# Kernel optimization log

Hardware: AMD Instinct MI355X
Metric: run time of the kernel (lower is better)

Reference implementation:

```python
import jax, jax.numpy as jnp
import numpy as np
import itertools, math

N_QUBITS = 16
HW_K = 8
N_LAYERS = 32
BATCH = 256
N_STATES = math.comb(N_QUBITS, HW_K)  # 12870


def _list_gates():
    gates = []
    for l in range(N_LAYERS):
        gates += [(q, q + 1) for q in range(l % 2, N_QUBITS - 1, 2)]
    return gates  # 240 gates


def _build_pairs(n, k, list_gates):
    # basis of Hamming-weight-k states, indexed as in map_RBS
    basis = list(itertools.combinations(range(n), k))
    idx = {s: i for i, s in enumerate(basis)}
    cache = {}
    rows = []
    for (i, j) in list_gates:
        if (i, j) not in cache:
            others = [q for q in range(n) if q != i and q != j]
            pr = []
            for s in itertools.combinations(others, k - 1):
                a = idx[tuple(sorted(s + (i,)))]
                b = idx[tuple(sorted(s + (j,)))]
                pr.append((a, b))
            cache[(i, j)] = pr
        rows.append(cache[(i, j)])
    return np.asarray(rows, dtype=np.int32)  # [G, P, 2], P = binom(n-2, k-1)


def setup_inputs() -> dict:
    key = jax.random.key(0)
    k1, k2 = jax.random.split(key)
    gates = _list_gates()
    pairs = jnp.asarray(_build_pairs(N_QUBITS, HW_K, gates))
    input_state = jax.random.normal(k1, (BATCH, N_STATES), dtype=jnp.float32)
    angles = jax.random.uniform(k2, (len(gates),), dtype=jnp.float32)  # nn.Parameter init torch.rand
    return {"input_state": input_state, "angles": angles, "pairs": pairs}


def reference(input_state, angles, pairs):
    # Each RBS gate applies, per affected pair (i, j) of basis states:
    #   y[i] =  cos(t) x[i] + sin(t) x[j]
    #   y[j] = -sin(t) x[i] + cos(t) x[j]
    # which is exactly (cos_matrix*cos + sin_matrix*sin + id_matrix) @ x.
    def step(state, gate):
        theta, pr = gate
        ii, jj = pr[:, 0], pr[:, 1]
        xi = state[:, ii]  # [B, P]
        xj = state[:, jj]
        c, s = jnp.cos(theta), jnp.sin(theta)
        state = state.at[:, ii].set(c * xi + s * xj)
        state = state.at[:, jj].set(c * xj - s * xi)
        return state, None

    out, _ = jax.lax.scan(step, input_state, (angles, pairs))
    return out
```

## Files before the change

### kernel.cpp

```cpp
#include <hip/hip_runtime.h>
#include <stdint.h>

#define NSTATES 12870
#define NPAD    15378
#define NPAIRS  3432
#define NGATES  240
#define PERIOD  15
#define NLP     16
#define TPB     1024

#define CS_OFF      0
#define BLK_OFF     1920
#define BLK_BYTES   23760
#define PU_ROWS     792
#define W2_ROWS     924
#define W2_SUB_OFF  12672
#define BND_OFF     96960
#define M2_OFF      4032
#define M1_OFF      14112
#define PERM_OFF    120000
#define WS_NEED     145740

__device__ __constant__ uint8_t OUTPOS[4][12] = {
  {4,5,6,7,8,9,10,11,12,13,14,15},
  {0,1,2,3,8,9,10,11,12,13,14,15},
  {0,1,2,3,4,5,6,7,12,13,14,15},
  {0,1,2,3,4,5,6,7,8,9,10,11}
};
__device__ __constant__ uint8_t FREEPOS[10] = {0,1,2,5,6,9,10,13,14,15};
__device__ __constant__ uint8_t IDPOS[16] = {0,1,2,3,4,5,6,7,8,9,10,11,12,13,14,15};
__device__ __constant__ uint8_t LRANK[16] = {0,0,1,0,2,1,2,0,3,3,4,1,5,2,3,0};
__device__ __constant__ uint8_t NBT[5]  = {1,4,6,4,1};
__device__ __constant__ uint8_t PPAD[5] = {1,5,7,5,1};

__global__ __launch_bounds__(256) void prep_fused(
    const float* __restrict__ angles, uint8_t* __restrict__ ws) {
  __shared__ int C[17][9];
  __shared__ int SECB[5][5][5];
  __shared__ int ROWB[5][5][13];
  if (threadIdx.x == 0) {
    for (int n = 0; n <= 16; ++n)
      for (int k = 0; k <= 8; ++k)
        C[n][k] = (k == 0) ? 1 : ((k > n) ? 0 : C[n-1][k-1] + C[n-1][k]);
    int acc = 0;
    for (int a0 = 0; a0 < 5; ++a0)
      for (int a1 = 0; a1 < 5; ++a1)
        for (int a2 = 0; a2 < 5; ++a2) {
          SECB[a0][a1][a2] = acc;
          int a3 = 8 - a0 - a1 - a2;
          if (a3 >= 0 && a3 <= 4) acc += NBT[a0] * NBT[a1] * NBT[a2] * PPAD[a3];
        }
  }
  for (int e = threadIdx.x; e < 325; e += 256) {
    int ow = e / 25, rem = e % 25, w0 = rem / 5, w1 = rem % 5;
    int base = 0;
    for (int c0 = 0; c0 < 5; ++c0)
      for (int c1 = 0; c1 < 5; ++c1) {
        int c2 = ow - c0 - c1;
        if (c2 < 0 || c2 > 4) continue;
        if (c0 < w0 || (c0 == w0 && c1 < w1)) base += NBT[c0] * NBT[c1] * NBT[c2];
      }
    ROWB[w0][w1][ow] = base;
  }
  __syncthreads();

  auto permof = [&](uint32_t mask) -> int {
    int g0 = mask & 15, g1 = (mask >> 4) & 15, g2 = (mask >> 8) & 15, g3 = (mask >> 12) & 15;
    int w0 = __popc(g0), w1 = __popc(g1), w2 = __popc(g2), w3 = __popc(g3);
    return SECB[w0][w1][w2] +
           ((LRANK[g0] * NBT[w1] + LRANK[g1]) * NBT[w2] + LRANK[g2]) * PPAD[w3] + LRANK[g3];
  };
  auto rowof = [&](int b, uint32_t mo) -> int {
    int wsx[3], lsx[3], ii = 0;
    for (int a = 0; a < 4; ++a) if (a != b) {
      int g = (mo >> (4 * a)) & 15;
      wsx[ii] = __popc(g); lsx[ii] = LRANK[g]; ++ii;
    }
    int outw = wsx[0] + wsx[1] + wsx[2];
    return ROWB[wsx[0]][wsx[1]][outw] +
           (lsx[0] * NBT[wsx[1]] + lsx[1]) * NBT[wsx[2]] + lsx[2];
  };
  auto unrank_mask = [&](int n, int k, int r, const uint8_t* pos) -> uint32_t {
    uint32_t m = 0; int v = 0;
    for (int i = 0; i < k; ++i) {
      for (;;) { int cnt = C[n - 1 - v][k - 1 - i]; if (r < cnt) break; r -= cnt; ++v; }
      m |= 1u << pos[v]; ++v;
    }
    return m;
  };

  int u = blockIdx.x * 256 + threadIdx.x;
  if (u < 10032) {
    int b = u / 2508, r = u % 2508;
    int p0 = 4 * b;
    uint32_t bmask = 0xFu << p0;
    uint8_t* blk = ws + BLK_OFF + b * BLK_BYTES;
    if (r < PU_ROWS) {
      uint32_t mo = unrank_mask(12, 7, r, OUTPOS[b]);
      int row = rowof(b, mo);
      uint32_t m0 = permof(mo | (1u << (p0 + 0)));
      uint32_t m1 = permof(mo | (1u << (p0 + 1)));
      uint32_t m2 = permof(mo | (1u << (p0 + 2)));
      uint32_t m3 = permof(mo | (1u << (p0 + 3)));
      uint32_t* pu = (uint32_t*)blk + (size_t)row * 4;
      pu[0] = m0 | (m1 << 16); pu[1] = m2 | (m3 << 16);
    } else if (r < PU_ROWS + W2_ROWS) {
      int o = r - PU_ROWS;
      uint32_t mo = unrank_mask(12, 6, o, OUTPOS[b]);
      int row = rowof(b, mo);
      const uint32_t pat[6] = {0x3u, 0x5u, 0x9u, 0x6u, 0xAu, 0xCu};
      uint32_t k0 = permof(mo | (pat[0] << p0)), k1 = permof(mo | (pat[1] << p0));
      uint32_t k2 = permof(mo | (pat[2] << p0)), k3 = permof(mo | (pat[3] << p0));
      uint32_t k4 = permof(mo | (pat[4] << p0)), k5 = permof(mo | (pat[5] << p0));
      uint32_t* w2 = (uint32_t*)(blk + W2_SUB_OFF) + (size_t)row * 3;
      w2[0] = k0 | (k1 << 16); w2[1] = k2 | (k3 << 16); w2[2] = k4 | (k5 << 16);
    } else {
      int o = r - PU_ROWS - W2_ROWS;
      uint32_t mo = unrank_mask(12, 5, o, OUTPOS[b]);
      int row = rowof(b, mo);
      uint32_t j0 = permof(mo | (bmask ^ (1u << (p0 + 0))));
      uint32_t j1 = permof(mo | (bmask ^ (1u << (p0 + 1))));
      uint32_t j2 = permof(mo | (bmask ^ (1u << (p0 + 2))));
      uint32_t j3 = permof(mo | (bmask ^ (1u << (p0 + 3))));
      uint32_t* pu = (uint32_t*)blk + (size_t)row * 4;
      pu[2] = j0 | (j1 << 16); pu[3] = j2 | (j3 << 16);
    }
  } else if (u < 13776) {
    int v = u - 10032;
    uint8_t* bnd = ws + BND_OFF;
    const uint32_t XL[3] = {1u << 3, 1u << 7, 1u << 11};
    const uint32_t XB[3] = {(1u<<3)|(1u<<4), (1u<<7)|(1u<<8), (1u<<11)|(1u<<12)};
    if (v < 252) {
      uint32_t mo = unrank_mask(10, 5, v, FREEPOS);
      uint32_t rep = mo | XL[0] | XL[1] | XL[2];
      uint32_t mm[8];
      for (int beta = 0; beta < 8; ++beta) {
        uint32_t m = rep;
        if (beta & 1) m ^= XB[0];
        if (beta & 2) m ^= XB[1];
        if (beta & 4) m ^= XB[2];
        mm[beta] = permof(m);
      }
      uint32_t* o = (uint32_t*)bnd + (size_t)v * 4;
      o[0] = mm[0] | (mm[1] << 16); o[1] = mm[2] | (mm[3] << 16);
      o[2] = mm[4] | (mm[5] << 16); o[3] = mm[6] | (mm[7] << 16);
    } else if (v < 1512) {
      int q = v - 252, cls = q / 420, o2 = q % 420;
      int gA = (cls == 2) ? 1 : 0;
      int gB = (cls == 0) ? 1 : 2;
      int gC = 3 - gA - gB;
      int vv = (o2 < 210) ? 0 : 1, oo = vv ? o2 - 210 : o2;
      uint32_t mo = unrank_mask(10, 6 - 2 * vv, oo, FREEPOS);
      uint32_t rep = mo | XL[gA] | XL[gB] | (vv ? XB[gC] : 0u);
      uint32_t mm[4];
      for (int beta = 0; beta < 4; ++beta) {
        uint32_t m = rep;
        if (beta & 1) m ^= XB[gA];
        if (beta & 2) m ^= XB[gB];
        mm[beta] = permof(m);
      }
      uint32_t* o = (uint32_t*)(bnd + M2_OFF + (size_t)cls * 3360) + (size_t)o2 * 2;
      o[0] = mm[0] | (mm[1] << 16); o[1] = mm[2] | (mm[3] << 16);
    } else {
      int q = v - 1512, cls = q / 744, o2 = q % 744;
      int ia = (cls == 0) ? 1 : 0;
      int ib = (cls == 2) ? 1 : 2;
      int v1, v2, f, oo;
      if      (o2 < 120) { v1 = 0; v2 = 0; f = 7; oo = o2; }
      else if (o2 < 372) { v1 = 0; v2 = 1; f = 5; oo = o2 - 120; }
      else if (o2 < 624) { v1 = 1; v2 = 0; f = 5; oo = o2 - 372; }
      else               { v1 = 1; v2 = 1; f = 3; oo = o2 - 624; }
      uint32_t mo = unrank_mask(10, f, oo, FREEPOS);
      uint32_t rep = mo | XL[cls] | (v1 ? XB[ia] : 0u) | (v2 ? XB[ib] : 0u);
      uint32_t m0 = permof(rep), m1 = permof(rep ^ XB[cls]);
      *((uint32_t*)(bnd + M1_OFF + (size_t)cls * 2976) + o2) = m0 | (m1 << 16);
    }
  } else if (u < 14016) {
    int g = u - 13776;
    float t = angles[g];
    ((float2*)(ws + CS_OFF))[g] = make_float2(cosf(t), sinf(t));
  } else if (u < 14016 + NSTATES) {
    int r = u - 14016;
    uint32_t mask = unrank_mask(16, 8, r, IDPOS);
    ((uint16_t*)(ws + PERM_OFF))[r] = (uint16_t)permof(mask);
  }
}

__device__ __forceinline__ void rot(float& rx, float& ry, const float2 cs) {
  float nx = fmaf(cs.x, rx, cs.y * ry);
  float ny = fmaf(cs.x, ry, -cs.y * rx);
  rx = nx; ry = ny;
}
__device__ __forceinline__ float lds_ld(const float* st, uint32_t boff) {
  return *(const float*)((const char*)st + boff);
}
__device__ __forceinline__ void lds_st(float* st, uint32_t boff, float v) {
  *(float*)((char*)st + boff) = v;
}

__global__ __launch_bounds__(TPB) void rbs_fused(
    const float* __restrict__ in, const uint8_t* __restrict__ ws,
    float* __restrict__ out) {
  __shared__ float st[NPAD];
  __shared__ float2 csl[NGATES];
  const int tid = threadIdx.x;
  const size_t row = blockIdx.x;
  const uint16_t* __restrict__ perm16 = (const uint16_t*)(ws + PERM_OFF);

  { const float* src = in + row * NSTATES;
    for (int i = tid; i < NSTATES; i += TPB) st[perm16[i]] = src[i]; }
  if (tid < NGATES) csl[tid] = ((const float2*)(ws + CS_OFF))[tid];

  const uint8_t* blkbase = ws + BLK_OFF;
  const uint8_t* bnd = ws + BND_OFF;
  const int w2id = (tid < 692) ? (tid + 232) : ((tid >= 792) ? (tid - 792) : -1);

  uint32_t o_i[4][4], o_j[4][4], o_k[4][6];
  if (tid < PU_ROWS) {
#pragma unroll
    for (int b = 0; b < 4; ++b) {
      uint4 mu = ((const uint4*)(blkbase + b * BLK_BYTES))[tid];
      o_i[b][0] = (mu.x & 0xffffu) << 2; o_i[b][1] = (mu.x >> 16) << 2;
      o_i[b][2] = (mu.y & 0xffffu) << 2; o_i[b][3] = (mu.y >> 16) << 2;
      o_j[b][0] = (mu.z & 0xffffu) << 2; o_j[b][1] = (mu.z >> 16) << 2;
      o_j[b][2] = (mu.w & 0xffffu) << 2; o_j[b][3] = (mu.w >> 16) << 2;
    }
  }
  if (w2id >= 0) {
#pragma unroll
    for (int b = 0; b < 4; ++b) {
      const uint32_t* p = (const uint32_t*)(blkbase + b * BLK_BYTES + W2_SUB_OFF) + (size_t)w2id * 3;
      uint32_t w0 = p[0], w1 = p[1], w2v = p[2];
      o_k[b][0] = (w0 & 0xffffu) << 2; o_k[b][1] = (w0 >> 16) << 2;
      o_k[b][2] = (w1 & 0xffffu) << 2; o_k[b][3] = (w1 >> 16) << 2;
      o_k[b][4] = (w2v & 0xffffu) << 2; o_k[b][5] = (w2v >> 16) << 2;
    }
  }
  uint4 bd[4];
#pragma unroll
  for (int k = 0; k < 4; ++k) {
    int u = tid + k * 1024;
    bd[k] = make_uint4(0u, 0u, 0u, 0u);
    if (u < 252) {
      bd[k] = ((const uint4*)bnd)[u];
    } else if (u < 1512) {
      int q = u - 252, cls = q / 420, o = q % 420;
      uint2 m = *(const uint2*)(bnd + M2_OFF + (size_t)cls * 3360 + (size_t)o * 8);
      bd[k].x = m.x; bd[k].y = m.y;
    } else if (u < 3744) {
      int q = u - 1512, cls = q / 744, o = q % 744;
      bd[k].x = *((const uint32_t*)(bnd + M1_OFF + (size_t)cls * 2976) + o);
    }
  }
  __syncthreads();

#pragma unroll 1
  for (int t = 0; t < NLP; ++t) {
    const int g0 = t * PERIOD;
#pragma unroll
    for (int b = 0; b < 4; ++b) {
      const float2 a1 = csl[g0 + 2 * b];
      const float2 a2 = csl[g0 + 2 * b + 1];
      const float2 a3 = csl[g0 + 8 + 2 * b];
      if (tid < PU_ROWS) {
        float x0 = lds_ld(st, o_i[b][0]), x1 = lds_ld(st, o_i[b][1]);
        float x2 = lds_ld(st, o_i[b][2]), x3 = lds_ld(st, o_i[b][3]);
        rot(x0, x1, a1); rot(x2, x3, a2); rot(x1, x2, a3);
        lds_st(st, o_i[b][0], x0); lds_st(st, o_i[b][1], x1);
        lds_st(st, o_i[b][2], x2); lds_st(st, o_i[b][3], x3);
        float y0 = lds_ld(st, o_j[b][0]), y1 = lds_ld(st, o_j[b][1]);
        float y2 = lds_ld(st, o_j[b][2]), y3 = lds_ld(st, o_j[b][3]);
        rot(y1, y0, a1); rot(y3, y2, a2); rot(y2, y1, a3);
        lds_st(st, o_j[b][0], y0); lds_st(st, o_j[b][1], y1);
        lds_st(st, o_j[b][2], y2); lds_st(st, o_j[b][3], y3);
      }
      if (w2id >= 0) {
        float z0 = lds_ld(st, o_k[b][0]), z1 = lds_ld(st, o_k[b][1]);
        float z2 = lds_ld(st, o_k[b][2]), z3 = lds_ld(st, o_k[b][3]);
        float z4 = lds_ld(st, o_k[b][4]), z5 = lds_ld(st, o_k[b][5]);
        rot(z1, z3, a1); rot(z2, z4, a1);
        rot(z1, z2, a2); rot(z3, z4, a2);
        rot(z0, z1, a3); rot(z4, z5, a3);
        lds_st(st, o_k[b][0], z0); lds_st(st, o_k[b][1], z1);
        lds_st(st, o_k[b][2], z2); lds_st(st, o_k[b][3], z3);
        lds_st(st, o_k[b][4], z4); lds_st(st, o_k[b][5], z5);
      }
      __syncthreads();
    }
    const float2 c0 = csl[g0 + 9], c1 = csl[g0 + 11], c2 = csl[g0 + 13];
#pragma unroll
    for (int k = 0; k < 4; ++k) {
      int u = tid + k * 1024;
      if (u >= 3744) break;
      uint4 d = bd[k];
      if (u < 252) {
        uint32_t e0 = (d.x & 0xffffu) << 2, e1 = (d.x >> 16) << 2;
        uint32_t e2 = (d.y & 0xffffu) << 2, e3 = (d.y >> 16) << 2;
        uint32_t e4 = (d.z & 0xffffu) << 2, e5 = (d.z >> 16) << 2;
        uint32_t e6 = (d.w & 0xffffu) << 2, e7 = (d.w >> 16) << 2;
        float x0 = lds_ld(st, e0), x1 = lds_ld(st, e1), x2 = lds_ld(st, e2), x3 = lds_ld(st, e3);
        float x4 = lds_ld(st, e4), x5 = lds_ld(st, e5), x6 = lds_ld(st, e6), x7 = lds_ld(st, e7);
        rot(x0, x1, c0); rot(x2, x3, c0); rot(x4, x5, c0); rot(x6, x7, c0);
        rot(x0, x2, c1); rot(x1, x3, c1); rot(x4, x6, c1); rot(x5, x7, c1);
        rot(x0, x4, c2); rot(x1, x5, c2); rot(x2, x6, c2); rot(x3, x7, c2);
        lds_st(st, e0, x0); lds_st(st, e1, x1); lds_st(st, e2, x2); lds_st(st, e3, x3);
        lds_st(st, e4, x4); lds_st(st, e5, x5); lds_st(st, e6, x6); lds_st(st, e7, x7);
      } else if (u < 1512) {
        int cls = (u - 252) / 420;
        float2 cA = (cls == 2) ? c1 : c0;
        float2 cB = (cls == 0) ? c1 : c2;
        uint32_t e0 = (d.x & 0xffffu) << 2, e1 = (d.x >> 16) << 2;
        uint32_t e2 = (d.y & 0xffffu) << 2, e3 = (d.y >> 16) << 2;
        float x0 = lds_ld(st, e0), x1 = lds_ld(st, e1), x2 = lds_ld(st, e2), x3 = lds_ld(st, e3);
        rot(x0, x1, cA); rot(x2, x3, cA);
        rot(x0, x2, cB); rot(x1, x3, cB);
        lds_st(st, e0, x0); lds_st(st, e1, x1); lds_st(st, e2, x2); lds_st(st, e3, x3);
      } else {
        int cls = (u - 1512) / 744;
        float2 cg = (cls == 0) ? c0 : ((cls == 1) ? c1 : c2);
        uint32_t e0 = (d.x & 0xffffu) << 2, e1 = (d.x >> 16) << 2;
        float x0 = lds_ld(st, e0), x1 = lds_ld(st, e1);
        rot(x0, x1, cg);
        lds_st(st, e0, x0); lds_st(st, e1, x1);
      }
    }
    __syncthreads();
  }

  { float* dst = out + row * NSTATES;
    for (int i = tid; i < NSTATES; i += TPB) dst[i] = st[perm16[i]]; }
}

__global__ __launch_bounds__(TPB) void rbs_raw(
    const float* __restrict__ in, const int* __restrict__ pairs_raw,
    const float* __restrict__ angles, float* __restrict__ out) {
  __shared__ float st[NSTATES];
  __shared__ float2 csl[NGATES];
  const int tid = threadIdx.x;
  const size_t row = blockIdx.x;
  const float* src = in + row * NSTATES;
  for (int i = tid; i < NSTATES; i += TPB) st[i] = src[i];
  for (int i = tid; i < NGATES; i += TPB) {
    float t = angles[i];
    csl[i] = make_float2(cosf(t), sinf(t));
  }
  __syncthreads();
  for (int g = 0; g < NGATES; ++g) {
    const float c = csl[g].x, s = csl[g].y;
    for (int p = tid; p < NPAIRS; p += TPB) {
      int2 ab = ((const int2*)pairs_raw)[(size_t)g * NPAIRS + p];
      float xi = st[ab.x], xj = st[ab.y];
      st[ab.x] = fmaf(c, xi, s * xj);
      st[ab.y] = fmaf(c, xj, -s * xi);
    }
    __syncthreads();
  }
  float* dst = out + row * NSTATES;
  for (int i = tid; i < NSTATES; i += TPB) dst[i] = st[i];
}

extern "C" void kernel_launch(void* const* d_in, const int* in_sizes, int n_in,
                              void* d_out, int out_size, void* d_ws, size_t ws_size,
                              hipStream_t stream) {
  const float* in = (const float*)d_in[0];
  const float* angles = (const float*)d_in[1];
  const int* pairs = (const int*)d_in[2];
  float* out = (float*)d_out;

  if (d_ws != nullptr && ws_size >= WS_NEED) {
    uint8_t* ws = (uint8_t*)d_ws;
    const int total = 14016 + NSTATES;
    prep_fused<<<(total + 255) / 256, 256, 0, stream>>>(angles, ws);
    rbs_fused<<<256, TPB, 0, stream>>>(in, ws, out);
  } else {
    rbs_raw<<<256, TPB, 0, stream>>>(in, pairs, angles, out);
  }
}
```

Baseline: 97.43 us.

## Fuse two 4-qubit blocks per pass with strided padded layout units

The per-block processing of the four 4-qubit groups (four passes, each with its own barrier) is replaced by two passes, each jointly mixing a pair of blocks (01, then 23). It uses a new padded LDS layout where the third axis is padded so each unit's addresses come from a base plus stride. Index tables shrink from per-element 16-bit offsets to one base/stride word per unit, which removes most workspace traffic and register-held offsets and halves the barriers in this phase. In exchange, the LDS footprint grows to about 73 KB of dynamic shared memory, and a deep branch tree dispatches 21 templated unit shapes with uneven per-thread work, which adds divergence.

```diff
diff --git a/kernel.cpp b/kernel.cpp
--- a/kernel.cpp
+++ b/kernel.cpp
@@ -2,42 +2,38 @@
 #include <stdint.h>
 
 #define NSTATES 12870
-#define NPAD    15378
-#define NPAIRS  3432
+#define NPAD2   18376
 #define NGATES  240
 #define PERIOD  15
 #define NLP     16
 #define TPB     1024
+#define NPAIRU  858
 
 #define CS_OFF      0
-#define BLK_OFF     1920
-#define BLK_BYTES   23760
-#define PU_ROWS     792
-#define W2_ROWS     924
-#define W2_SUB_OFF  12672
-#define BND_OFF     96960
+#define P01_OFF     1920
+#define P23_OFF     5352
+#define BND_OFF     8784
 #define M2_OFF      4032
 #define M1_OFF      14112
-#define PERM_OFF    120000
-#define WS_NEED     145740
-
-__device__ __constant__ uint8_t OUTPOS[4][12] = {
-  {4,5,6,7,8,9,10,11,12,13,14,15},
-  {0,1,2,3,8,9,10,11,12,13,14,15},
-  {0,1,2,3,4,5,6,7,12,13,14,15},
-  {0,1,2,3,4,5,6,7,8,9,10,11}
-};
+#define PERM_OFF    31824
+#define WS_NEED     57564
+#define DYNLDS      (NPAD2 * 4)
+
 __device__ __constant__ uint8_t FREEPOS[10] = {0,1,2,5,6,9,10,13,14,15};
 __device__ __constant__ uint8_t IDPOS[16] = {0,1,2,3,4,5,6,7,8,9,10,11,12,13,14,15};
 __device__ __constant__ uint8_t LRANK[16] = {0,0,1,0,2,1,2,0,3,3,4,1,5,2,3,0};
 __device__ __constant__ uint8_t NBT[5]  = {1,4,6,4,1};
 __device__ __constant__ uint8_t PPAD[5] = {1,5,7,5,1};
+__device__ __constant__ uint8_t PAX2[5] = {1,5,7,5,1};
+__device__ __constant__ uint8_t  CLSW0[21] = {0,4,0,4,0,4, 1,1,2,2,3,3, 1,1,1, 2,2,2, 3,3,3};
+__device__ __constant__ uint8_t  CLSW1[21] = {1,1,2,2,3,3, 0,4,0,4,0,4, 1,2,3, 1,2,3, 1,2,3};
+__device__ __constant__ uint16_t CLSS[22] =
+  {0,8,64,92,120,176,184,192,248,276,304,360,368,396,452,522,578,648,704,774,830,858};
 
 __global__ __launch_bounds__(256) void prep_fused(
     const float* __restrict__ angles, uint8_t* __restrict__ ws) {
   __shared__ int C[17][9];
   __shared__ int SECB[5][5][5];
-  __shared__ int ROWB[5][5][13];
   if (threadIdx.x == 0) {
     for (int n = 0; n <= 16; ++n)
       for (int k = 0; k <= 8; ++k)
@@ -48,19 +44,8 @@
         for (int a2 = 0; a2 < 5; ++a2) {
           SECB[a0][a1][a2] = acc;
           int a3 = 8 - a0 - a1 - a2;
-          if (a3 >= 0 && a3 <= 4) acc += NBT[a0] * NBT[a1] * NBT[a2] * PPAD[a3];
+          if (a3 >= 0 && a3 <= 4) acc += NBT[a0] * NBT[a1] * PAX2[a2] * PPAD[a3];
         }
-  }
-  for (int e = threadIdx.x; e < 325; e += 256) {
-    int ow = e / 25, rem = e % 25, w0 = rem / 5, w1 = rem % 5;
-    int base = 0;
-    for (int c0 = 0; c0 < 5; ++c0)
-      for (int c1 = 0; c1 < 5; ++c1) {
-        int c2 = ow - c0 - c1;
-        if (c2 < 0 || c2 > 4) continue;
-        if (c0 < w0 || (c0 == w0 && c1 < w1)) base += NBT[c0] * NBT[c1] * NBT[c2];
-      }
-    ROWB[w0][w1][ow] = base;
   }
   __syncthreads();
 
@@ -68,17 +53,7 @@
     int g0 = mask & 15, g1 = (mask >> 4) & 15, g2 = (mask >> 8) & 15, g3 = (mask >> 12) & 15;
     int w0 = __popc(g0), w1 = __popc(g1), w2 = __popc(g2), w3 = __popc(g3);
     return SECB[w0][w1][w2] +
-           ((LRANK[g0] * NBT[w1] + LRANK[g1]) * NBT[w2] + LRANK[g2]) * PPAD[w3] + LRANK[g3];
-  };
-  auto rowof = [&](int b, uint32_t mo) -> int {
-    int wsx[3], lsx[3], ii = 0;
-    for (int a = 0; a < 4; ++a) if (a != b) {
-      int g = (mo >> (4 * a)) & 15;
-      wsx[ii] = __popc(g); lsx[ii] = LRANK[g]; ++ii;
-    }
-    int outw = wsx[0] + wsx[1] + wsx[2];
-    return ROWB[wsx[0]][wsx[1]][outw] +
-           (lsx[0] * NBT[wsx[1]] + lsx[1]) * NBT[wsx[2]] + lsx[2];
+           ((LRANK[g0] * NBT[w1] + LRANK[g1]) * PAX2[w2] + LRANK[g2]) * PPAD[w3] + LRANK[g3];
   };
   auto unrank_mask = [&](int n, int k, int r, const uint8_t* pos) -> uint32_t {
     uint32_t m = 0; int v = 0;
@@ -90,43 +65,32 @@
   };
 
   int u = blockIdx.x * 256 + threadIdx.x;
-  if (u < 10032) {
-    int b = u / 2508, r = u % 2508;
-    int p0 = 4 * b;
-    uint32_t bmask = 0xFu << p0;
-    uint8_t* blk = ws + BLK_OFF + b * BLK_BYTES;
-    if (r < PU_ROWS) {
-      uint32_t mo = unrank_mask(12, 7, r, OUTPOS[b]);
-      int row = rowof(b, mo);
-      uint32_t m0 = permof(mo | (1u << (p0 + 0)));
-      uint32_t m1 = permof(mo | (1u << (p0 + 1)));
-      uint32_t m2 = permof(mo | (1u << (p0 + 2)));
-      uint32_t m3 = permof(mo | (1u << (p0 + 3)));
-      uint32_t* pu = (uint32_t*)blk + (size_t)row * 4;
-      pu[0] = m0 | (m1 << 16); pu[1] = m2 | (m3 << 16);
-    } else if (r < PU_ROWS + W2_ROWS) {
-      int o = r - PU_ROWS;
-      uint32_t mo = unrank_mask(12, 6, o, OUTPOS[b]);
-      int row = rowof(b, mo);
-      const uint32_t pat[6] = {0x3u, 0x5u, 0x9u, 0x6u, 0xAu, 0xCu};
-      uint32_t k0 = permof(mo | (pat[0] << p0)), k1 = permof(mo | (pat[1] << p0));
-      uint32_t k2 = permof(mo | (pat[2] << p0)), k3 = permof(mo | (pat[3] << p0));
-      uint32_t k4 = permof(mo | (pat[4] << p0)), k5 = permof(mo | (pat[5] << p0));
-      uint32_t* w2 = (uint32_t*)(blk + W2_SUB_OFF) + (size_t)row * 3;
-      w2[0] = k0 | (k1 << 16); w2[1] = k2 | (k3 << 16); w2[2] = k4 | (k5 << 16);
+  if (u < 2 * NPAIRU) {
+    const bool is01 = (u < NPAIRU);
+    const int uu = is01 ? u : u - NPAIRU;
+    int c = 0;
+    while (c < 20 && uu >= (int)CLSS[c + 1]) ++c;
+    int r = uu - CLSS[c];
+    const int wa = CLSW0[c], wb = CLSW1[c];
+    const int W = 8 - wa - wb;
+    int wc = 0, wd = 0, lc = 0, ld = 0;
+    for (wc = 0; wc <= 4; ++wc) {
+      wd = W - wc; if (wd < 0 || wd > 4) continue;
+      int n = NBT[wc] * NBT[wd];
+      if (r < n) { lc = r / NBT[wd]; ld = r % NBT[wd]; break; }
+      r -= n;
+    }
+    if (is01) {
+      int base = SECB[wa][wb][wc] + lc * PPAD[wd] + ld;
+      int strd = PAX2[wc] * PPAD[wd];
+      ((uint32_t*)(ws + P01_OFF))[uu] = (uint32_t)base | ((uint32_t)strd << 16);
     } else {
-      int o = r - PU_ROWS - W2_ROWS;
-      uint32_t mo = unrank_mask(12, 5, o, OUTPOS[b]);
-      int row = rowof(b, mo);
-      uint32_t j0 = permof(mo | (bmask ^ (1u << (p0 + 0))));
-      uint32_t j1 = permof(mo | (bmask ^ (1u << (p0 + 1))));
-      uint32_t j2 = permof(mo | (bmask ^ (1u << (p0 + 2))));
-      uint32_t j3 = permof(mo | (bmask ^ (1u << (p0 + 3))));
-      uint32_t* pu = (uint32_t*)blk + (size_t)row * 4;
-      pu[2] = j0 | (j1 << 16); pu[3] = j2 | (j3 << 16);
-    }
-  } else if (u < 13776) {
-    int v = u - 10032;
+      int base = SECB[wc][wd][wa] + (lc * NBT[wd] + ld) * PAX2[wa] * PPAD[wb];
+      int pstr = PPAD[wb];
+      ((uint32_t*)(ws + P23_OFF))[uu] = (uint32_t)base | ((uint32_t)pstr << 16);
+    }
+  } else if (u < 2 * NPAIRU + 3744) {
+    int v = u - 2 * NPAIRU;
     uint8_t* bnd = ws + BND_OFF;
     const uint32_t XL[3] = {1u << 3, 1u << 7, 1u << 11};
     const uint32_t XB[3] = {(1u<<3)|(1u<<4), (1u<<7)|(1u<<8), (1u<<11)|(1u<<12)};
@@ -175,12 +139,12 @@
       uint32_t m0 = permof(rep), m1 = permof(rep ^ XB[cls]);
       *((uint32_t*)(bnd + M1_OFF + (size_t)cls * 2976) + o2) = m0 | (m1 << 16);
     }
-  } else if (u < 14016) {
-    int g = u - 13776;
+  } else if (u < 2 * NPAIRU + 3744 + NGATES) {
+    int g = u - (2 * NPAIRU + 3744);
     float t = angles[g];
     ((float2*)(ws + CS_OFF))[g] = make_float2(cosf(t), sinf(t));
-  } else if (u < 14016 + NSTATES) {
-    int r = u - 14016;
+  } else if (u < 2 * NPAIRU + 3744 + NGATES + NSTATES) {
+    int r = u - (2 * NPAIRU + 3744 + NGATES);
     uint32_t mask = unrank_mask(16, 8, r, IDPOS);
     ((uint16_t*)(ws + PERM_OFF))[r] = (uint16_t)permof(mask);
   }
@@ -198,10 +162,92 @@
   *(float*)((char*)st + boff) = v;
 }
 
-__global__ __launch_bounds__(TPB) void rbs_fused(
+template<int W, int S>
+__device__ __forceinline__ void mix_axis(float* x, const float2 a1, const float2 a2, const float2 a3) {
+  if constexpr (W == 1) {
+    rot(x[0], x[S], a1); rot(x[2*S], x[3*S], a2); rot(x[S], x[2*S], a3);
+  } else if constexpr (W == 2) {
+    rot(x[S], x[2*S], a1);   rot(x[3*S], x[4*S], a1);
+    rot(x[S], x[3*S], a2);   rot(x[2*S], x[4*S], a2);
+    rot(x[0], x[S], a3);     rot(x[4*S], x[5*S], a3);
+  } else if constexpr (W == 3) {
+    rot(x[2*S], x[3*S], a1); rot(x[0], x[S], a2); rot(x[S], x[2*S], a3);
+  }
+}
+
+template<int KA, int KB>
+__device__ __forceinline__ void do_unit(float* st, uint32_t base, uint32_t sA, uint32_t sB,
+    const float2 a1, const float2 a2, const float2 a3,
+    const float2 b1, const float2 b2, const float2 b3) {
+  constexpr int NA = (KA == 0) ? 1 : ((KA == 2) ? 6 : 4);
+  constexpr int NB = (KB == 0) ? 1 : ((KB == 2) ? 6 : 4);
+  float x[NA * NB];
+#pragma unroll
+  for (int ia = 0; ia < NA; ++ia)
+#pragma unroll
+    for (int ib = 0; ib < NB; ++ib)
+      x[ia * NB + ib] = lds_ld(st, base + ia * sA + ib * sB);
+  if constexpr (KA != 0) {
+#pragma unroll
+    for (int ib = 0; ib < NB; ++ib) mix_axis<KA, NB>(&x[ib], a1, a2, a3);
+  }
+  if constexpr (KB != 0) {
+#pragma unroll
+    for (int ia = 0; ia < NA; ++ia) mix_axis<KB, 1>(&x[ia * NB], b1, b2, b3);
+  }
+#pragma unroll
+  for (int ia = 0; ia < NA; ++ia)
+#pragma unroll
+    for (int ib = 0; ib < NB; ++ib)
+      lds_st(st, base + ia * sA + ib * sB, x[ia * NB + ib]);
+}
+
+template<int KA, int KB, bool LIN>
+__device__ __forceinline__ void run_unit(float* st, uint32_t md,
+    const float2 a1, const float2 a2, const float2 a3,
+    const float2 b1, const float2 b2, const float2 b3) {
+  constexpr int NB = (KB == 0) ? 1 : ((KB == 2) ? 6 : 4);
+  const uint32_t base = (md & 0xffffu) << 2;
+  uint32_t sA, sB;
+  if constexpr (LIN) { sB = (md >> 16) << 2; sA = NB * sB; }
+  else               { sA = (md >> 16) << 2; sB = 4; }
+  do_unit<KA, KB>(st, base, sA, sB, a1, a2, a3, b1, b2, b3);
+}
+
+template<bool LIN>
+__device__ __forceinline__ void dispatch_pair(int tid, float* st, uint32_t md,
+    const float2 a1, const float2 a2, const float2 a3,
+    const float2 b1, const float2 b2, const float2 b3) {
+  if (tid < 368) {
+    if (tid < 184) {
+      if (tid < 64)       run_unit<0,1,LIN>(st, md, a1,a2,a3, b1,b2,b3);
+      else if (tid < 120) run_unit<0,2,LIN>(st, md, a1,a2,a3, b1,b2,b3);
+      else                run_unit<0,3,LIN>(st, md, a1,a2,a3, b1,b2,b3);
+    } else {
+      if (tid < 248)      run_unit<1,0,LIN>(st, md, a1,a2,a3, b1,b2,b3);
+      else if (tid < 304) run_unit<2,0,LIN>(st, md, a1,a2,a3, b1,b2,b3);
+      else                run_unit<3,0,LIN>(st, md, a1,a2,a3, b1,b2,b3);
+    }
+  } else {
+    if (tid < 578) {
+      if (tid < 396)      run_unit<1,1,LIN>(st, md, a1,a2,a3, b1,b2,b3);
+      else if (tid < 452) run_unit<1,2,LIN>(st, md, a1,a2,a3, b1,b2,b3);
+      else if (tid < 522) run_unit<1,3,LIN>(st, md, a1,a2,a3, b1,b2,b3);
+      else                run_unit<2,1,LIN>(st, md, a1,a2,a3, b1,b2,b3);
+    } else {
+      if (tid < 648)      run_unit<2,2,LIN>(st, md, a1,a2,a3, b1,b2,b3);
+      else if (tid < 704) run_unit<2,3,LIN>(st, md, a1,a2,a3, b1,b2,b3);
+      else if (tid < 774) run_unit<3,1,LIN>(st, md, a1,a2,a3, b1,b2,b3);
+      else if (tid < 830) run_unit<3,2,LIN>(st, md, a1,a2,a3, b1,b2,b3);
+      else                run_unit<3,3,LIN>(st, md, a1,a2,a3, b1,b2,b3);
+    }
+  }
+}
+
+__global__ __launch_bounds__(TPB) void rbs_fused2(
     const float* __restrict__ in, const uint8_t* __restrict__ ws,
     float* __restrict__ out) {
-  __shared__ float st[NPAD];
+  extern __shared__ float st[];
   __shared__ float2 csl[NGATES];
   const int tid = threadIdx.x;
   const size_t row = blockIdx.x;
@@ -211,31 +257,9 @@
     for (int i = tid; i < NSTATES; i += TPB) st[perm16[i]] = src[i]; }
   if (tid < NGATES) csl[tid] = ((const float2*)(ws + CS_OFF))[tid];
 
-  const uint8_t* blkbase = ws + BLK_OFF;
+  const uint32_t md01 = (tid < NPAIRU) ? ((const uint32_t*)(ws + P01_OFF))[tid] : 0u;
+  const uint32_t md23 = (tid < NPAIRU) ? ((const uint32_t*)(ws + P23_OFF))[tid] : 0u;
   const uint8_t* bnd = ws + BND_OFF;
-  const int w2id = (tid < 692) ? (tid + 232) : ((tid >= 792) ? (tid - 792) : -1);
-
-  uint32_t o_i[4][4], o_j[4][4], o_k[4][6];
-  if (tid < PU_ROWS) {
-#pragma unroll
-    for (int b = 0; b < 4; ++b) {
-      uint4 mu = ((const uint4*)(blkbase + b * BLK_BYTES))[tid];
-      o_i[b][0] = (mu.x & 0xffffu) << 2; o_i[b][1] = (mu.x >> 16) << 2;
-      o_i[b][2] = (mu.y & 0xffffu) << 2; o_i[b][3] = (mu.y >> 16) << 2;
-      o_j[b][0] = (mu.z & 0xffffu) << 2; o_j[b][1] = (mu.z >> 16) << 2;
-      o_j[b][2] = (mu.w & 0xffffu) << 2; o_j[b][3] = (mu.w >> 16) << 2;
-    }
-  }
-  if (w2id >= 0) {
-#pragma unroll
-    for (int b = 0; b < 4; ++b) {
-      const uint32_t* p = (const uint32_t*)(blkbase + b * BLK_BYTES + W2_SUB_OFF) + (size_t)w2id * 3;
-      uint32_t w0 = p[0], w1 = p[1], w2v = p[2];
-      o_k[b][0] = (w0 & 0xffffu) << 2; o_k[b][1] = (w0 >> 16) << 2;
-      o_k[b][2] = (w1 & 0xffffu) << 2; o_k[b][3] = (w1 >> 16) << 2;
-      o_k[b][4] = (w2v & 0xffffu) << 2; o_k[b][5] = (w2v >> 16) << 2;
-    }
-  }
   uint4 bd[4];
 #pragma unroll
   for (int k = 0; k < 4; ++k) {
@@ -257,36 +281,14 @@
 #pragma unroll 1
   for (int t = 0; t < NLP; ++t) {
     const int g0 = t * PERIOD;
-#pragma unroll
-    for (int b = 0; b < 4; ++b) {
-      const float2 a1 = csl[g0 + 2 * b];
-      const float2 a2 = csl[g0 + 2 * b + 1];
-      const float2 a3 = csl[g0 + 8 + 2 * b];
-      if (tid < PU_ROWS) {
-        float x0 = lds_ld(st, o_i[b][0]), x1 = lds_ld(st, o_i[b][1]);
-        float x2 = lds_ld(st, o_i[b][2]), x3 = lds_ld(st, o_i[b][3]);
-        rot(x0, x1, a1); rot(x2, x3, a2); rot(x1, x2, a3);
-        lds_st(st, o_i[b][0], x0); lds_st(st, o_i[b][1], x1);
-        lds_st(st, o_i[b][2], x2); lds_st(st, o_i[b][3], x3);
-        float y0 = lds_ld(st, o_j[b][0]), y1 = lds_ld(st, o_j[b][1]);
-        float y2 = lds_ld(st, o_j[b][2]), y3 = lds_ld(st, o_j[b][3]);
-        rot(y1, y0, a1); rot(y3, y2, a2); rot(y2, y1, a3);
-        lds_st(st, o_j[b][0], y0); lds_st(st, o_j[b][1], y1);
-        lds_st(st, o_j[b][2], y2); lds_st(st, o_j[b][3], y3);
-      }
-      if (w2id >= 0) {
-        float z0 = lds_ld(st, o_k[b][0]), z1 = lds_ld(st, o_k[b][1]);
-        float z2 = lds_ld(st, o_k[b][2]), z3 = lds_ld(st, o_k[b][3]);
-        float z4 = lds_ld(st, o_k[b][4]), z5 = lds_ld(st, o_k[b][5]);
-        rot(z1, z3, a1); rot(z2, z4, a1);
-        rot(z1, z2, a2); rot(z3, z4, a2);
-        rot(z0, z1, a3); rot(z4, z5, a3);
-        lds_st(st, o_k[b][0], z0); lds_st(st, o_k[b][1], z1);
-        lds_st(st, o_k[b][2], z2); lds_st(st, o_k[b][3], z3);
-        lds_st(st, o_k[b][4], z4); lds_st(st, o_k[b][5], z5);
-      }
-      __syncthreads();
-    }
+    if (tid < NPAIRU)
+      dispatch_pair<true>(tid, st, md01,
+          csl[g0], csl[g0+1], csl[g0+8], csl[g0+2], csl[g0+3], csl[g0+10]);
+    __syncthreads();
+    if (tid < NPAIRU)
+      dispatch_pair<false>(tid, st, md23,
+          csl[g0+4], csl[g0+5], csl[g0+12], csl[g0+6], csl[g0+7], csl[g0+14]);
+    __syncthreads();
     const float2 c0 = csl[g0 + 9], c1 = csl[g0 + 11], c2 = csl[g0 + 13];
 #pragma unroll
     for (int k = 0; k < 4; ++k) {
@@ -334,12 +336,12 @@
 __global__ __launch_bounds__(TPB) void rbs_raw(
     const float* __restrict__ in, const int* __restrict__ pairs_raw,
     const float* __restrict__ angles, float* __restrict__ out) {
-  __shared__ float st[NSTATES];
+  __shared__ float stx[NSTATES];
   __shared__ float2 csl[NGATES];
   const int tid = threadIdx.x;
   const size_t row = blockIdx.x;
   const float* src = in + row * NSTATES;
-  for (int i = tid; i < NSTATES; i += TPB) st[i] = src[i];
+  for (int i = tid; i < NSTATES; i += TPB) stx[i] = src[i];
   for (int i = tid; i < NGATES; i += TPB) {
     float t = angles[i];
     csl[i] = make_float2(cosf(t), sinf(t));
@@ -347,16 +349,16 @@
   __syncthreads();
   for (int g = 0; g < NGATES; ++g) {
     const float c = csl[g].x, s = csl[g].y;
-    for (int p = tid; p < NPAIRS; p += TPB) {
-      int2 ab = ((const int2*)pairs_raw)[(size_t)g * NPAIRS + p];
-      float xi = st[ab.x], xj = st[ab.y];
-      st[ab.x] = fmaf(c, xi, s * xj);
-      st[ab.y] = fmaf(c, xj, -s * xi);
+    for (int p = tid; p < 3432; p += TPB) {
+      int2 ab = ((const int2*)pairs_raw)[(size_t)g * 3432 + p];
+      float xi = stx[ab.x], xj = stx[ab.y];
+      stx[ab.x] = fmaf(c, xi, s * xj);
+      stx[ab.y] = fmaf(c, xj, -s * xi);
     }
     __syncthreads();
   }
   float* dst = out + row * NSTATES;
-  for (int i = tid; i < NSTATES; i += TPB) dst[i] = st[i];
+  for (int i = tid; i < NSTATES; i += TPB) dst[i] = stx[i];
 }
 
 extern "C" void kernel_launch(void* const* d_in, const int* in_sizes, int n_in,
@@ -369,9 +371,11 @@
 
   if (d_ws != nullptr && ws_size >= WS_NEED) {
     uint8_t* ws = (uint8_t*)d_ws;
-    const int total = 14016 + NSTATES;
+    (void)hipFuncSetAttribute((const void*)rbs_fused2,
+                              hipFuncAttributeMaxDynamicSharedMemorySize, DYNLDS);
+    const int total = 2 * NPAIRU + 3744 + NGATES + NSTATES;
     prep_fused<<<(total + 255) / 256, 256, 0, stream>>>(angles, ws);
-    rbs_fused<<<256, TPB, 0, stream>>>(in, ws, out);
+    rbs_fused2<<<256, TPB, DYNLDS, stream>>>(in, ws, out);
   } else {
     rbs_raw<<<256, TPB, 0, stream>>>(in, pairs, angles, out);
   }
```

Result: slower. 110.9 us (+13.8%).
